# Performance work log

Measured on AMD Instinct MI355X. Metric: run time of the kernel, lower is better.

The kernel has to match this reference:

```python
import jax, jax.numpy as jnp
import numpy as np

BATCH, SIZE_IN, SIZE_OUT = 2048, 256, 512


def setup_inputs() -> dict:
    key = jax.random.key(0)
    kx, ka = jax.random.split(key)
    x = jax.random.normal(kx, (BATCH, SIZE_IN), dtype=jnp.float32)
    A = jax.random.normal(ka, (SIZE_IN, SIZE_OUT), dtype=jnp.float32)
    return {"x": x, "A": A}


def reference(x, A):
    # W = sigmoid(A): [size_in, size_out]
    W = jax.nn.sigmoid(A)
    # tropical (max-times) matmul: out[i,k] = max_j W[j,k] * x[i,j]
    # broadcast [B,1,J_in->axis1]... x: [B,J,1], W: [1,J,K] -> [B,J,K] -> max over J
    out = jnp.max(x[:, :, None] * W[None, :, :], axis=1)  # [B, K]
    return out
```

## Files before the change

### kernel.cpp

```cpp
#include <hip/hip_runtime.h>
#include <math.h>


constexpr int BATCH = 2048;
constexpr int JDIM  = 256;
constexpr int KDIM  = 512;

constexpr int BI  = 64;
constexpr int BK  = 64;
constexpr int JC  = 64;
constexpr int NCH = JDIM / JC;
constexpr int PAD = 68;

__device__ __forceinline__ float sigmoidf_fast(float a) {
    return 1.0f / (1.0f + __expf(-a));
}

__global__ __launch_bounds__(256) void tropical_mm_kernel(
        const float* __restrict__ x,
        const float* __restrict__ A,
        float* __restrict__ out) {
    __shared__ float xT[JC][PAD];
    __shared__ float Wt[JC][PAD];

    const int tid = threadIdx.x;
    const int tx  = tid & 15;
    const int ty  = tid >> 4;
    const int bk  = blockIdx.x & 7;
    const int bi  = blockIdx.x >> 3;
    const int i0  = bi * BI;
    const int k0  = bk * BK;

    float4 px[4], pa[4];

    {
        const int jb = 0;
        #pragma unroll
        for (int p = 0; p < 4; ++p) {
            const int iL = p * 16 + ty;
            const int jL = p * 16 + ty;
            px[p] = *(const float4*)&x[(i0 + iL) * JDIM + jb + tx * 4];
            pa[p] = *(const float4*)&A[(jb + jL) * KDIM + k0 + tx * 4];
        }
    }

    float acc[4][4];
    #pragma unroll
    for (int a = 0; a < 4; ++a)
        #pragma unroll
        for (int b = 0; b < 4; ++b)
            acc[a][b] = -__builtin_inff();

    const int ty4 = ty * 4;
    const int tx4 = tx * 4;

    for (int c = 0; c < NCH; ++c) {
        __syncthreads();

        #pragma unroll
        for (int p = 0; p < 4; ++p) {
            const int iL = p * 16 + ty;
            xT[tx4 + 0][iL] = px[p].x;
            xT[tx4 + 1][iL] = px[p].y;
            xT[tx4 + 2][iL] = px[p].z;
            xT[tx4 + 3][iL] = px[p].w;

            const int jL = p * 16 + ty;
            float4 w;
            w.x = sigmoidf_fast(pa[p].x);
            w.y = sigmoidf_fast(pa[p].y);
            w.z = sigmoidf_fast(pa[p].z);
            w.w = sigmoidf_fast(pa[p].w);
            *(float4*)&Wt[jL][tx4] = w;
        }
        __syncthreads();

        if (c + 1 < NCH) {
            const int jb = (c + 1) * JC;
            #pragma unroll
            for (int p = 0; p < 4; ++p) {
                const int iL = p * 16 + ty;
                const int jL = p * 16 + ty;
                px[p] = *(const float4*)&x[(i0 + iL) * JDIM + jb + tx * 4];
                pa[p] = *(const float4*)&A[(jb + jL) * KDIM + k0 + tx * 4];
            }
        }

        #pragma unroll 4
        for (int j = 0; j < JC; j += 2) {
            const float4 xv0 = *(const float4*)&xT[j][ty4];
            const float4 wv0 = *(const float4*)&Wt[j][tx4];
            const float4 xv1 = *(const float4*)&xT[j + 1][ty4];
            const float4 wv1 = *(const float4*)&Wt[j + 1][tx4];
            const float x0[4] = {xv0.x, xv0.y, xv0.z, xv0.w};
            const float w0[4] = {wv0.x, wv0.y, wv0.z, wv0.w};
            const float x1[4] = {xv1.x, xv1.y, xv1.z, xv1.w};
            const float w1[4] = {wv1.x, wv1.y, wv1.z, wv1.w};
            #pragma unroll
            for (int a = 0; a < 4; ++a)
                #pragma unroll
                for (int b = 0; b < 4; ++b)
                    acc[a][b] = fmaxf(fmaxf(x0[a] * w0[b], x1[a] * w1[b]), acc[a][b]);
        }
    }

    #pragma unroll
    for (int a = 0; a < 4; ++a) {
        float4 o;
        o.x = acc[a][0];
        o.y = acc[a][1];
        o.z = acc[a][2];
        o.w = acc[a][3];
        *(float4*)&out[(i0 + ty4 + a) * KDIM + k0 + tx4] = o;
    }
}

extern "C" void kernel_launch(void* const* d_in, const int* in_sizes, int n_in,
                              void* d_out, int out_size, void* d_ws, size_t ws_size,
                              hipStream_t stream) {
    const float* x = (const float*)d_in[0];
    const float* A = (const float*)d_in[1];
    float* out = (float*)d_out;

    dim3 grid(256);
    dim3 block(256);
    hipLaunchKernelGGL(tropical_mm_kernel, grid, block, 0, stream, x, A, out);
}
```

Baseline: 26.51 us.

## Precompute sigmoid weights and switch to per-wave register tiling without LDS

Adds a separate kernel that applies sigmoid to A once and writes W to the workspace, so the main kernel no longer recomputes it in every block. The main kernel drops shared memory and barriers: each wave owns 8 batch rows by 64 output columns, keeps W in double-buffered registers loaded from global memory, and reads x as wave-uniform float4 loads. This removes LDS traffic and syncs but cuts per-thread reuse to 8 outputs, adds a second launch, and relies on cache for repeated x and W reads.

```diff
diff --git a/kernel.cpp b/kernel.cpp
--- a/kernel.cpp
+++ b/kernel.cpp
@@ -1,118 +1,82 @@
 #include <hip/hip_runtime.h>
-#include <math.h>
 
 
 constexpr int BATCH = 2048;
-constexpr int JDIM  = 256;
-constexpr int KDIM  = 512;
+constexpr int JD    = 256;
+constexpr int KD    = 512;
 
-constexpr int BI  = 64;
-constexpr int BK  = 64;
-constexpr int JC  = 64;
-constexpr int NCH = JDIM / JC;
-constexpr int PAD = 68;
+constexpr int TI = 8;
+constexpr int JC = 32;
 
 __device__ __forceinline__ float sigmoidf_fast(float a) {
     return 1.0f / (1.0f + __expf(-a));
 }
 
+__global__ __launch_bounds__(256) void sigmoid_pre(const float* __restrict__ A,
+                                                   float* __restrict__ W) {
+    const int idx = (blockIdx.x * 256 + threadIdx.x) * 4;
+    float4 a = *(const float4*)(A + idx);
+    float4 w;
+    w.x = sigmoidf_fast(a.x);
+    w.y = sigmoidf_fast(a.y);
+    w.z = sigmoidf_fast(a.z);
+    w.w = sigmoidf_fast(a.w);
+    *(float4*)(W + idx) = w;
+}
+
 __global__ __launch_bounds__(256) void tropical_mm_kernel(
         const float* __restrict__ x,
-        const float* __restrict__ A,
+        const float* __restrict__ W,
         float* __restrict__ out) {
-    __shared__ float xT[JC][PAD];
-    __shared__ float Wt[JC][PAD];
+    const int wslot = __builtin_amdgcn_readfirstlane((int)(threadIdx.x >> 6));
+    const int wid   = (int)blockIdx.x * 4 + wslot;
+    const int lane  = (int)(threadIdx.x & 63);
 
-    const int tid = threadIdx.x;
-    const int tx  = tid & 15;
-    const int ty  = tid >> 4;
-    const int bk  = blockIdx.x & 7;
-    const int bi  = blockIdx.x >> 3;
-    const int i0  = bi * BI;
-    const int k0  = bk * BK;
+    const int i0 = (wid >> 3) * TI;
+    const int k  = ((wid & 7) << 6) + lane;
 
-    float4 px[4], pa[4];
+    const float* Wk = W + k;
 
-    {
-        const int jb = 0;
+    float acc[TI];
+    #pragma unroll
+    for (int i = 0; i < TI; ++i) acc[i] = -__builtin_inff();
+
+    float wa[JC], wb[JC];
+
+    auto loadw = [&](float (&w)[JC], int jc) {
+        const float* p = Wk + jc * KD;
         #pragma unroll
-        for (int p = 0; p < 4; ++p) {
-            const int iL = p * 16 + ty;
-            const int jL = p * 16 + ty;
-            px[p] = *(const float4*)&x[(i0 + iL) * JDIM + jb + tx * 4];
-            pa[p] = *(const float4*)&A[(jb + jL) * KDIM + k0 + tx * 4];
-        }
-    }
+        for (int j = 0; j < JC; ++j) w[j] = p[j * KD];
+    };
 
-    float acc[4][4];
-    #pragma unroll
-    for (int a = 0; a < 4; ++a)
+    auto compute = [&](const float (&w)[JC], int jc) {
         #pragma unroll
-        for (int b = 0; b < 4; ++b)
-            acc[a][b] = -__builtin_inff();
-
-    const int ty4 = ty * 4;
-    const int tx4 = tx * 4;
-
-    for (int c = 0; c < NCH; ++c) {
-        __syncthreads();
-
-        #pragma unroll
-        for (int p = 0; p < 4; ++p) {
-            const int iL = p * 16 + ty;
-            xT[tx4 + 0][iL] = px[p].x;
-            xT[tx4 + 1][iL] = px[p].y;
-            xT[tx4 + 2][iL] = px[p].z;
-            xT[tx4 + 3][iL] = px[p].w;
-
-            const int jL = p * 16 + ty;
-            float4 w;
-            w.x = sigmoidf_fast(pa[p].x);
-            w.y = sigmoidf_fast(pa[p].y);
-            w.z = sigmoidf_fast(pa[p].z);
-            w.w = sigmoidf_fast(pa[p].w);
-            *(float4*)&Wt[jL][tx4] = w;
-        }
-        __syncthreads();
-
-        if (c + 1 < NCH) {
-            const int jb = (c + 1) * JC;
+        for (int i = 0; i < TI; ++i) {
+            const float4* xr = (const float4*)(x + (i0 + i) * JD + jc);
             #pragma unroll
-            for (int p = 0; p < 4; ++p) {
-                const int iL = p * 16 + ty;
-                const int jL = p * 16 + ty;
-                px[p] = *(const float4*)&x[(i0 + iL) * JDIM + jb + tx * 4];
-                pa[p] = *(const float4*)&A[(jb + jL) * KDIM + k0 + tx * 4];
+            for (int q = 0; q < JC / 4; ++q) {
+                const float4 xv = xr[q];
+                acc[i] = fmaxf(fmaxf(xv.x * w[4 * q + 0],
+                                     xv.y * w[4 * q + 1]), acc[i]);
+                acc[i] = fmaxf(fmaxf(xv.z * w[4 * q + 2],
+                                     xv.w * w[4 * q + 3]), acc[i]);
             }
         }
+    };
 
-        #pragma unroll 4
-        for (int j = 0; j < JC; j += 2) {
-            const float4 xv0 = *(const float4*)&xT[j][ty4];
-            const float4 wv0 = *(const float4*)&Wt[j][tx4];
-            const float4 xv1 = *(const float4*)&xT[j + 1][ty4];
-            const float4 wv1 = *(const float4*)&Wt[j + 1][tx4];
-            const float x0[4] = {xv0.x, xv0.y, xv0.z, xv0.w};
-            const float w0[4] = {wv0.x, wv0.y, wv0.z, wv0.w};
-            const float x1[4] = {xv1.x, xv1.y, xv1.z, xv1.w};
-            const float w1[4] = {wv1.x, wv1.y, wv1.z, wv1.w};
-            #pragma unroll
-            for (int a = 0; a < 4; ++a)
-                #pragma unroll
-                for (int b = 0; b < 4; ++b)
-                    acc[a][b] = fmaxf(fmaxf(x0[a] * w0[b], x1[a] * w1[b]), acc[a][b]);
-        }
+    loadw(wa, 0);
+    for (int c = 0; c < JD / JC; c += 2) {
+        const int jc0 = c * JC;
+        const int jc1 = jc0 + JC;
+        const int jc2 = jc0 + 2 * JC;
+        if (jc1 < JD) loadw(wb, jc1);
+        compute(wa, jc0);
+        if (jc2 < JD) loadw(wa, jc2);
+        if (jc1 < JD) compute(wb, jc1);
     }
 
     #pragma unroll
-    for (int a = 0; a < 4; ++a) {
-        float4 o;
-        o.x = acc[a][0];
-        o.y = acc[a][1];
-        o.z = acc[a][2];
-        o.w = acc[a][3];
-        *(float4*)&out[(i0 + ty4 + a) * KDIM + k0 + tx4] = o;
-    }
+    for (int i = 0; i < TI; ++i) out[(i0 + i) * KD + k] = acc[i];
 }
 
 extern "C" void kernel_launch(void* const* d_in, const int* in_sizes, int n_in,
@@ -121,8 +85,10 @@
     const float* x = (const float*)d_in[0];
     const float* A = (const float*)d_in[1];
     float* out = (float*)d_out;
+    float* W   = (float*)d_ws;
 
-    dim3 grid(256);
-    dim3 block(256);
-    hipLaunchKernelGGL(tropical_mm_kernel, grid, block, 0, stream, x, A, out);
+    hipLaunchKernelGGL(sigmoid_pre, dim3(128), dim3(256), 0, stream, A, W);
+
+    hipLaunchKernelGGL(tropical_mm_kernel, dim3(512), dim3(256), 0, stream,
+                       x, W, out);
 }
```

Result: slower. 39.19 us (+47.8%).
